# Kernel optimization log

Measured on AMD Instinct MI355X. Metric: run time of the kernel, lower is better.

The kernel has to match this reference:

```python
import jax, jax.numpy as jnp
import numpy as np

B, S, D, E, K, H = 2, 1024, 1024, 8, 2, 2048
Z_COEF = 1e-4  # router_z_loss_coef


def setup_inputs() -> dict:
    key = jax.random.key(0)
    ks = jax.random.split(key, 9)
    std = 0.02
    return {
        "x": jax.random.normal(ks[0], (B, S, D), jnp.float32),
        "router_w": jax.random.normal(ks[1], (E, D), jnp.float32) * std,
        "router_bias": jnp.zeros((E,), jnp.float32),
        "gate_w": jax.random.normal(ks[2], (E, H, D), jnp.float32) * std,
        "up_w": jax.random.normal(ks[3], (E, H, D), jnp.float32) * std,
        "down_w": jax.random.normal(ks[4], (E, D, H), jnp.float32) * std,
        "sh_gate_w": jax.random.normal(ks[5], (H, D), jnp.float32) * std,
        "sh_up_w": jax.random.normal(ks[6], (H, D), jnp.float32) * std,
        "sh_down_w": jax.random.normal(ks[7], (D, H), jnp.float32) * std,
    }


def reference(x, router_w, router_bias, gate_w, up_w, down_w, sh_gate_w, sh_up_w, sh_down_w):
    b, s, d = x.shape
    flat = x.reshape(-1, d)                                   # [N, D]
    n_tokens = flat.shape[0]

    # ---- router ----
    logits = flat @ router_w.T                                # [N, E]
    biased = logits + jax.lax.stop_gradient(router_bias)      # bias is detached
    _, topk_idx = jax.lax.top_k(biased, K)                    # [N, K]
    topk_logits = jnp.take_along_axis(logits, topk_idx, axis=-1)
    topk_weights = jax.nn.softmax(topk_logits.astype(jnp.float32), axis=-1).astype(x.dtype)

    router_z = jax.nn.logsumexp(logits.astype(jnp.float32), axis=-1)
    router_z_loss = jnp.mean(router_z ** 2) * Z_COEF

    # ---- load-balance stats (detached in the original via no_grad) ----
    full_probs = jax.lax.stop_gradient(jax.nn.softmax(logits.astype(jnp.float32), axis=-1))
    p_i = full_probs.mean(axis=0)                             # [E]
    mask = jnp.zeros_like(full_probs).at[jnp.arange(n_tokens)[:, None], topk_idx].set(1.0)
    f_i = mask.mean(axis=0)                                   # [E]
    load_balance = jnp.sum(p_i * f_i) * E
    aux_loss = jnp.zeros((), x.dtype)                         # load_balancing == "aux_loss_free"

    # ---- routed experts ----
    # Identical math to gather(weights)[token] + SwiGLU einsum + scatter-add:
    # out[n] = sum_k w[n,k] * SwiGLU_{idx[n,k]}(x[n]), computed as E masked GEMMs
    # to avoid materializing [N*K, H, D] weight copies.
    routed = jnp.zeros_like(flat)
    for e in range(E):
        w_e = jnp.sum(topk_weights * (topk_idx == e), axis=-1)            # [N]
        h = jax.nn.silu(flat @ gate_w[e].T) * (flat @ up_w[e].T)          # [N, H]
        routed = routed + w_e[:, None] * (h @ down_w[e].T)                # [N, D]

    # ---- shared expert (num_shared_experts = 1) ----
    shared = (jax.nn.silu(flat @ sh_gate_w.T) * (flat @ sh_up_w.T)) @ sh_down_w.T

    hidden_states = (routed + shared).reshape(b, s, d)
    return hidden_states, aux_loss, router_z_loss, jax.lax.stop_gradient(load_balance)
```

## Files before the change

kernel.cpp:

```cpp
#include <hip/hip_runtime.h>

#define N_TOK 2048
#define DIM   1024
#define NE    8
#define HID   2048
#define A_SHARED 4096
#define OUT_HID (N_TOK * DIM)

typedef float v4f __attribute__((ext_vector_type(4)));
typedef short v8s __attribute__((ext_vector_type(8)));

#define OFF_XBF   0ull
#define OFF_H     4194304ull
#define OFF_GW    29360128ull
#define OFF_UW    67108864ull
#define OFF_DW    104857600ull
#define OFF_TOK   142606336ull
#define OFF_WL    (OFF_TOK + 24576ull)
#define OFF_IDX   (OFF_WL + 24576ull)
#define OFF_TW    (OFF_IDX + 16384ull)
#define OFF_STATS (OFF_TW + 16384ull)

struct Stats {
  int counts[NE];
  int fill[NE];
  int offs[NE + 2];
  float z2;
  float psum[NE];
};

__device__ __forceinline__ unsigned short f2bf(float f) {
  union { float f; unsigned u; } v; v.f = f;
  unsigned r = v.u + 0x7FFFu + ((v.u >> 16) & 1u);
  return (unsigned short)(r >> 16);
}
__device__ __forceinline__ unsigned pack2bf(float a, float b) {
  return (unsigned)f2bf(a) | ((unsigned)f2bf(b) << 16);
}

__device__ __forceinline__ void async_lds16(const void* g, void* l) {
  __builtin_amdgcn_global_load_lds(
      (const __attribute__((address_space(1))) void*)g,
      (__attribute__((address_space(3))) void*)l, 16, 0, 0);
}

#define REG_F8 2359296u
#define EXP_F8 2097152u
__global__ __launch_bounds__(256) void cast_w_kernel(
    const float* __restrict__ g, const float* __restrict__ u, const float* __restrict__ dn,
    const float* __restrict__ shg, const float* __restrict__ shu, const float* __restrict__ shd,
    unsigned short* __restrict__ outw) {
  unsigned r = blockIdx.y;
  unsigned j = blockIdx.x * 256 + threadIdx.x;
  const float* eb = (r == 0) ? g : (r == 1) ? u : dn;
  const float* sb = (r == 0) ? shg : (r == 1) ? shu : shd;
  const float* src = (j < EXP_F8) ? eb + 8ull * j : sb + 8ull * (j - EXP_F8);
  float4 a = ((const float4*)src)[0];
  float4 b = ((const float4*)src)[1];
  uint4 o;
  o.x = pack2bf(a.x, a.y);
  o.y = pack2bf(a.z, a.w);
  o.z = pack2bf(b.x, b.y);
  o.w = pack2bf(b.z, b.w);
  ((uint4*)outw)[(size_t)r * REG_F8 + j] = o;
}

__global__ __launch_bounds__(256) void router_kernel(
    const float* __restrict__ x, const float* __restrict__ rw, const float* __restrict__ rb,
    unsigned short* __restrict__ xbf,
    int* __restrict__ idxbuf, float* __restrict__ twbuf, Stats* __restrict__ st) {
  int lane = threadIdx.x & 63;
  int wv = threadIdx.x >> 6;
  int n = blockIdx.x * 4 + wv;

  float acc[NE];
#pragma unroll
  for (int e = 0; e < NE; ++e) acc[e] = 0.f;

  const float4* x4 = (const float4*)(x + (size_t)n * DIM);
  uint2* xb2 = (uint2*)xbf + (size_t)n * 256;
#pragma unroll
  for (int q = 0; q < 4; ++q) {
    float4 xv = x4[q * 64 + lane];
    uint2 xo;
    xo.x = pack2bf(xv.x, xv.y);
    xo.y = pack2bf(xv.z, xv.w);
    xb2[q * 64 + lane] = xo;
#pragma unroll
    for (int e = 0; e < NE; ++e) {
      const float4* w4 = (const float4*)(rw + (size_t)e * DIM);
      float4 wvv = w4[q * 64 + lane];
      acc[e] += xv.x * wvv.x + xv.y * wvv.y + xv.z * wvv.z + xv.w * wvv.w;
    }
  }
#pragma unroll
  for (int off = 32; off; off >>= 1) {
#pragma unroll
    for (int e = 0; e < NE; ++e) acc[e] += __shfl_xor(acc[e], off);
  }

  float mx = acc[0];
#pragma unroll
  for (int e = 1; e < NE; ++e) mx = fmaxf(mx, acc[e]);
  float pr[NE];
  float es = 0.f;
#pragma unroll
  for (int e = 0; e < NE; ++e) { pr[e] = __expf(acc[e] - mx); es += pr[e]; }
  float inv = 1.f / es;
#pragma unroll
  for (int e = 0; e < NE; ++e) pr[e] *= inv;
  float z = mx + __logf(es);

  float b0 = -1e30f; int i0 = 0;
#pragma unroll
  for (int e = 0; e < NE; ++e) {
    float bb = acc[e] + rb[e];
    if (bb > b0) { b0 = bb; i0 = e; }
  }
  float b1 = -1e30f; int i1 = 0;
#pragma unroll
  for (int e = 0; e < NE; ++e) {
    if (e == i0) continue;
    float bb = acc[e] + rb[e];
    if (bb > b1) { b1 = bb; i1 = e; }
  }
  float l0 = acc[i0], l1 = acc[i1];
  float m2 = fmaxf(l0, l1);
  float e0 = __expf(l0 - m2), e1 = __expf(l1 - m2);
  float den = 1.f / (e0 + e1);
  float w0 = e0 * den, w1 = e1 * den;

  __shared__ float redp[4][9];
  __shared__ int redc[4][8];
  if (lane == 0) {
    idxbuf[n * 2] = i0; idxbuf[n * 2 + 1] = i1;
    twbuf[n * 2] = w0;  twbuf[n * 2 + 1] = w1;
#pragma unroll
    for (int e = 0; e < NE; ++e) redp[wv][e] = pr[e];
    redp[wv][8] = z * z;
#pragma unroll
    for (int e = 0; e < NE; ++e) redc[wv][e] = (e == i0) + (e == i1);
  }
  __syncthreads();
  int t = threadIdx.x;
  if (t < 9) {
    float s = redp[0][t] + redp[1][t] + redp[2][t] + redp[3][t];
    if (t < 8) atomicAdd(&st->psum[t], s);
    else       atomicAdd(&st->z2, s);
  } else if (t >= 16 && t < 24) {
    int e = t - 16;
    atomicAdd(&st->counts[e], redc[0][e] + redc[1][e] + redc[2][e] + redc[3][e]);
  }
}

__global__ void scan_kernel(Stats* __restrict__ st, float* __restrict__ out) {
  if (threadIdx.x == 0 && blockIdx.x == 0) {
    int o = 0;
#pragma unroll
    for (int e = 0; e < NE; ++e) { st->offs[e] = o; o += st->counts[e]; }
    st->offs[NE] = o;
    st->offs[NE + 1] = o + N_TOK;
    float zl = st->z2 / (float)N_TOK * 1e-4f;
    float lb = 0.f;
#pragma unroll
    for (int e = 0; e < NE; ++e)
      lb += (st->psum[e] / (float)N_TOK) * ((float)st->counts[e] / (float)N_TOK);
    lb *= (float)NE;
    out[OUT_HID + 0] = 0.f;
    out[OUT_HID + 1] = zl;
    out[OUT_HID + 2] = lb;
  }
}

__global__ __launch_bounds__(256) void scatter_kernel(
    const int* __restrict__ idxbuf, const float* __restrict__ twbuf,
    Stats* __restrict__ st, int* __restrict__ tok, float* __restrict__ wl) {
  int n = blockIdx.x * 256 + threadIdx.x;
#pragma unroll
  for (int k = 0; k < 2; ++k) {
    int e = idxbuf[n * 2 + k];
    int pos = st->offs[e] + atomicAdd(&st->fill[e], 1);
    tok[pos] = n;
    wl[pos] = twbuf[n * 2 + k];
  }
  tok[A_SHARED + n] = n;
  wl[A_SHARED + n] = 1.f;
}


__global__ __launch_bounds__(256, 2) void gateup_kernel(
    const unsigned short* __restrict__ gwbf, const unsigned short* __restrict__ uwbf,
    const unsigned short* __restrict__ xbf, const int* __restrict__ tok,
    const Stats* __restrict__ st, unsigned short* __restrict__ hbuf) {
  int e = blockIdx.z;
  int seg0 = st->offs[e];
  int cnt = st->offs[e + 1] - seg0;
  int m0 = blockIdx.y * 128;
  if (m0 >= cnt) return;
  int n0 = blockIdx.x * 128;

  __shared__ alignas(16) unsigned short As[2][128 * 32];
  __shared__ alignas(16) unsigned short Bg[2][128 * 32];
  __shared__ alignas(16) unsigned short Bu[2][128 * 32];

  int tid = threadIdx.x, l = tid & 63, w = tid >> 6;
  int wr = w >> 1, wc = w & 1;

  int sj = l >> 3;
  int ss = (l & 7) ^ sj;
  int grow = 2 * sj + (ss >> 2);
  int gch = ss & 3;

  const unsigned short* ap[2];
  const unsigned short* gp[2];
  const unsigned short* up[2];
#pragma unroll
  for (int q = 0; q < 2; ++q) {
    int row = (w * 2 + q) * 16 + grow;
    int ar = m0 + row; if (ar > cnt - 1) ar = cnt - 1;
    ap[q] = xbf + (size_t)tok[seg0 + ar] * DIM + gch * 8;
    size_t wb = (size_t)e * HID * DIM + (size_t)(n0 + row) * DIM + gch * 8;
    gp[q] = gwbf + wb;
    up[q] = uwbf + wb;
  }

  int lh = (l & 15) >> 1;
  int lofs = lh * 64 + ((((l & 1) * 4 + (l >> 4)) ^ lh) * 8);

  v4f accg[4][4], accu[4][4];
#pragma unroll
  for (int mi = 0; mi < 4; ++mi)
#pragma unroll
    for (int ni = 0; ni < 4; ++ni) {
      accg[mi][ni] = (v4f){0.f, 0.f, 0.f, 0.f};
      accu[mi][ni] = (v4f){0.f, 0.f, 0.f, 0.f};
    }

#pragma unroll
  for (int q = 0; q < 2; ++q) {
    async_lds16(ap[q], &As[0][(w * 2 + q) * 512]);
    async_lds16(gp[q], &Bg[0][(w * 2 + q) * 512]);
    async_lds16(up[q], &Bu[0][(w * 2 + q) * 512]);
  }

  int pb = 0;
  for (int k0 = 0; k0 < DIM; k0 += 32, pb ^= 1) {
    __syncthreads();

    v8s af[4], bgf[4], buf_[4];
#pragma unroll
    for (int mi = 0; mi < 4; ++mi)
      af[mi] = *(const v8s*)&As[pb][(wr * 32 + mi * 8) * 64 + lofs];
#pragma unroll
    for (int ni = 0; ni < 4; ++ni) {
      bgf[ni]  = *(const v8s*)&Bg[pb][(wc * 32 + ni * 8) * 64 + lofs];
      buf_[ni] = *(const v8s*)&Bu[pb][(wc * 32 + ni * 8) * 64 + lofs];
    }

    if (k0 + 32 < DIM) {
      int nb = pb ^ 1;
      int kn = k0 + 32;
#pragma unroll
      for (int q = 0; q < 2; ++q) {
        async_lds16(ap[q] + kn, &As[nb][(w * 2 + q) * 512]);
        async_lds16(gp[q] + kn, &Bg[nb][(w * 2 + q) * 512]);
        async_lds16(up[q] + kn, &Bu[nb][(w * 2 + q) * 512]);
      }
    }

#pragma unroll
    for (int mi = 0; mi < 4; ++mi)
#pragma unroll
      for (int ni = 0; ni < 4; ++ni) {
        accg[mi][ni] = __builtin_amdgcn_mfma_f32_16x16x32_bf16(af[mi], bgf[ni], accg[mi][ni], 0, 0, 0);
        accu[mi][ni] = __builtin_amdgcn_mfma_f32_16x16x32_bf16(af[mi], buf_[ni], accu[mi][ni], 0, 0, 0);
      }
  }

  int col = l & 15, rq = (l >> 4) * 4;
#pragma unroll
  for (int mi = 0; mi < 4; ++mi) {
#pragma unroll
    for (int rr = 0; rr < 4; ++rr) {
      int rl = wr * 64 + mi * 16 + rq + rr;
      if (m0 + rl < cnt) {
        size_t rowb = (size_t)(seg0 + m0 + rl) * HID + n0 + wc * 64;
#pragma unroll
        for (int ni = 0; ni < 4; ++ni) {
          float g = accg[mi][ni][rr], u = accu[mi][ni][rr];
          hbuf[rowb + ni * 16 + col] = f2bf(g * u / (1.f + __expf(-g)));
        }
      }
    }
  }
}

__global__ __launch_bounds__(256, 2) void down_kernel(
    const unsigned short* __restrict__ dwbf, const unsigned short* __restrict__ hbuf,
    const int* __restrict__ tok, const float* __restrict__ wl,
    const Stats* __restrict__ st, float* __restrict__ out) {
  int e = blockIdx.z;
  int seg0 = st->offs[e];
  int cnt = st->offs[e + 1] - seg0;
  int m0 = blockIdx.y * 128;
  if (m0 >= cnt) return;
  int n0 = blockIdx.x * 128;

  __shared__ alignas(16) unsigned short As[2][128 * 32];
  __shared__ alignas(16) unsigned short Bs[2][128 * 32];

  int tid = threadIdx.x, l = tid & 63, w = tid >> 6;
  int wr = w >> 1, wc = w & 1;

  int sj = l >> 3;
  int ss = (l & 7) ^ sj;
  int grow = 2 * sj + (ss >> 2);
  int gch = ss & 3;

  const unsigned short* ap[2];
  const unsigned short* bp[2];
#pragma unroll
  for (int q = 0; q < 2; ++q) {
    int row = (w * 2 + q) * 16 + grow;
    int ar = m0 + row; if (ar > cnt - 1) ar = cnt - 1;
    ap[q] = hbuf + (size_t)(seg0 + ar) * HID + gch * 8;
    bp[q] = dwbf + (size_t)e * DIM * HID + (size_t)(n0 + row) * HID + gch * 8;
  }

  int lh = (l & 15) >> 1;
  int lofs = lh * 64 + ((((l & 1) * 4 + (l >> 4)) ^ lh) * 8);

  v4f acc[4][4];
#pragma unroll
  for (int mi = 0; mi < 4; ++mi)
#pragma unroll
    for (int ni = 0; ni < 4; ++ni) acc[mi][ni] = (v4f){0.f, 0.f, 0.f, 0.f};

#pragma unroll
  for (int q = 0; q < 2; ++q) {
    async_lds16(ap[q], &As[0][(w * 2 + q) * 512]);
    async_lds16(bp[q], &Bs[0][(w * 2 + q) * 512]);
  }

  int pb = 0;
  for (int k0 = 0; k0 < HID; k0 += 32, pb ^= 1) {
    __syncthreads();

    v8s af[4], bf[4];
#pragma unroll
    for (int mi = 0; mi < 4; ++mi)
      af[mi] = *(const v8s*)&As[pb][(wr * 32 + mi * 8) * 64 + lofs];
#pragma unroll
    for (int ni = 0; ni < 4; ++ni)
      bf[ni] = *(const v8s*)&Bs[pb][(wc * 32 + ni * 8) * 64 + lofs];

    if (k0 + 32 < HID) {
      int nb = pb ^ 1;
      int kn = k0 + 32;
#pragma unroll
      for (int q = 0; q < 2; ++q) {
        async_lds16(ap[q] + kn, &As[nb][(w * 2 + q) * 512]);
        async_lds16(bp[q] + kn, &Bs[nb][(w * 2 + q) * 512]);
      }
    }

#pragma unroll
    for (int mi = 0; mi < 4; ++mi)
#pragma unroll
      for (int ni = 0; ni < 4; ++ni)
        acc[mi][ni] = __builtin_amdgcn_mfma_f32_16x16x32_bf16(af[mi], bf[ni], acc[mi][ni], 0, 0, 0);
  }

  int col = l & 15, rq = (l >> 4) * 4;
#pragma unroll
  for (int mi = 0; mi < 4; ++mi) {
#pragma unroll
    for (int rr = 0; rr < 4; ++rr) {
      int rl = wr * 64 + mi * 16 + rq + rr;
      if (m0 + rl < cnt) {
        int t = tok[seg0 + m0 + rl];
        float wgt = wl[seg0 + m0 + rl];
        float* ob = out + (size_t)t * DIM + n0 + wc * 64;
#pragma unroll
        for (int ni = 0; ni < 4; ++ni)
          atomicAdd(ob + ni * 16 + col, acc[mi][ni][rr] * wgt);
      }
    }
  }
}

extern "C" void kernel_launch(void* const* d_in, const int* in_sizes, int n_in,
                              void* d_out, int out_size, void* d_ws, size_t ws_size,
                              hipStream_t stream) {
  const float* x   = (const float*)d_in[0];
  const float* rw  = (const float*)d_in[1];
  const float* rb  = (const float*)d_in[2];
  const float* gw  = (const float*)d_in[3];
  const float* uw  = (const float*)d_in[4];
  const float* dw  = (const float*)d_in[5];
  const float* shg = (const float*)d_in[6];
  const float* shu = (const float*)d_in[7];
  const float* shd = (const float*)d_in[8];
  float* out = (float*)d_out;
  char* ws = (char*)d_ws;

  unsigned short* xbf  = (unsigned short*)(ws + OFF_XBF);
  unsigned short* hbuf = (unsigned short*)(ws + OFF_H);
  unsigned short* gwbf = (unsigned short*)(ws + OFF_GW);
  unsigned short* uwbf = (unsigned short*)(ws + OFF_UW);
  unsigned short* dwbf = (unsigned short*)(ws + OFF_DW);
  int*   tok  = (int*)(ws + OFF_TOK);
  float* wl   = (float*)(ws + OFF_WL);
  int*   idxb = (int*)(ws + OFF_IDX);
  float* twb  = (float*)(ws + OFF_TW);
  Stats* st   = (Stats*)(ws + OFF_STATS);

  hipMemsetAsync(d_out, 0, (size_t)out_size * sizeof(float), stream);
  hipMemsetAsync(st, 0, sizeof(Stats), stream);

  cast_w_kernel<<<dim3(9216, 3), 256, 0, stream>>>(gw, uw, dw, shg, shu, shd, gwbf);
  router_kernel<<<512, 256, 0, stream>>>(x, rw, rb, xbf, idxb, twb, st);
  scan_kernel<<<1, 64, 0, stream>>>(st, out);
  scatter_kernel<<<8, 256, 0, stream>>>(idxb, twb, st, tok, wl);
  gateup_kernel<<<dim3(16, 16, 9), 256, 0, stream>>>(gwbf, uwbf, xbf, tok, st, hbuf);
  down_kernel<<<dim3(8, 16, 9), 256, 0, stream>>>(dwbf, hbuf, tok, wl, st, out);
}
```

Measured before the change: 418.1 us.

## Fuse fp32-to-bf16 weight cast into GEMM tile loads, drop cast kernel

```diff
diff --git a/kernel.cpp b/kernel.cpp
--- a/kernel.cpp
+++ b/kernel.cpp
@@ -12,10 +12,7 @@
 
 #define OFF_XBF   0ull
 #define OFF_H     4194304ull
-#define OFF_GW    29360128ull
-#define OFF_UW    67108864ull
-#define OFF_DW    104857600ull
-#define OFF_TOK   142606336ull
+#define OFF_TOK   29360128ull
 #define OFF_WL    (OFF_TOK + 24576ull)
 #define OFF_IDX   (OFF_WL + 24576ull)
 #define OFF_TW    (OFF_IDX + 16384ull)
@@ -38,31 +35,24 @@
   return (unsigned)f2bf(a) | ((unsigned)f2bf(b) << 16);
 }
 
+__device__ __forceinline__ unsigned cvt2bf(float a, float b) {
+  unsigned r;
+  asm("v_cvt_pk_bf16_f32 %0, %1, %2" : "=v"(r) : "v"(a), "v"(b));
+  return r;
+}
+__device__ __forceinline__ void st8bf(unsigned short* p, float4 a, float4 b) {
+  uint4 o;
+  o.x = cvt2bf(a.x, a.y);
+  o.y = cvt2bf(a.z, a.w);
+  o.z = cvt2bf(b.x, b.y);
+  o.w = cvt2bf(b.z, b.w);
+  *(uint4*)p = o;
+}
+
 __device__ __forceinline__ void async_lds16(const void* g, void* l) {
   __builtin_amdgcn_global_load_lds(
       (const __attribute__((address_space(1))) void*)g,
       (__attribute__((address_space(3))) void*)l, 16, 0, 0);
-}
-
-#define REG_F8 2359296u
-#define EXP_F8 2097152u
-__global__ __launch_bounds__(256) void cast_w_kernel(
-    const float* __restrict__ g, const float* __restrict__ u, const float* __restrict__ dn,
-    const float* __restrict__ shg, const float* __restrict__ shu, const float* __restrict__ shd,
-    unsigned short* __restrict__ outw) {
-  unsigned r = blockIdx.y;
-  unsigned j = blockIdx.x * 256 + threadIdx.x;
-  const float* eb = (r == 0) ? g : (r == 1) ? u : dn;
-  const float* sb = (r == 0) ? shg : (r == 1) ? shu : shd;
-  const float* src = (j < EXP_F8) ? eb + 8ull * j : sb + 8ull * (j - EXP_F8);
-  float4 a = ((const float4*)src)[0];
-  float4 b = ((const float4*)src)[1];
-  uint4 o;
-  o.x = pack2bf(a.x, a.y);
-  o.y = pack2bf(a.z, a.w);
-  o.z = pack2bf(b.x, b.y);
-  o.w = pack2bf(b.z, b.w);
-  ((uint4*)outw)[(size_t)r * REG_F8 + j] = o;
 }
 
 __global__ __launch_bounds__(256) void router_kernel(
@@ -189,7 +179,8 @@
 
 
 __global__ __launch_bounds__(256, 2) void gateup_kernel(
-    const unsigned short* __restrict__ gwbf, const unsigned short* __restrict__ uwbf,
+    const float* __restrict__ gw, const float* __restrict__ uw,
+    const float* __restrict__ shg, const float* __restrict__ shu,
     const unsigned short* __restrict__ xbf, const int* __restrict__ tok,
     const Stats* __restrict__ st, unsigned short* __restrict__ hbuf) {
   int e = blockIdx.z;
@@ -211,17 +202,20 @@
   int grow = 2 * sj + (ss >> 2);
   int gch = ss & 3;
 
+  const float* gbase = (e < NE) ? gw + (size_t)e * HID * DIM : shg;
+  const float* ubase = (e < NE) ? uw + (size_t)e * HID * DIM : shu;
+
   const unsigned short* ap[2];
-  const unsigned short* gp[2];
-  const unsigned short* up[2];
+  const float* gp[2];
+  const float* up[2];
 #pragma unroll
   for (int q = 0; q < 2; ++q) {
     int row = (w * 2 + q) * 16 + grow;
     int ar = m0 + row; if (ar > cnt - 1) ar = cnt - 1;
     ap[q] = xbf + (size_t)tok[seg0 + ar] * DIM + gch * 8;
-    size_t wb = (size_t)e * HID * DIM + (size_t)(n0 + row) * DIM + gch * 8;
-    gp[q] = gwbf + wb;
-    up[q] = uwbf + wb;
+    size_t wb = (size_t)(n0 + row) * DIM + gch * 8;
+    gp[q] = gbase + wb;
+    up[q] = ubase + wb;
   }
 
   int lh = (l & 15) >> 1;
@@ -236,11 +230,21 @@
       accu[mi][ni] = (v4f){0.f, 0.f, 0.f, 0.f};
     }
 
+  float4 rg[2][2], ru[2][2];
 #pragma unroll
   for (int q = 0; q < 2; ++q) {
+    rg[q][0] = ((const float4*)gp[q])[0];
+    rg[q][1] = ((const float4*)gp[q])[1];
+    ru[q][0] = ((const float4*)up[q])[0];
+    ru[q][1] = ((const float4*)up[q])[1];
+  }
+#pragma unroll
+  for (int q = 0; q < 2; ++q)
     async_lds16(ap[q], &As[0][(w * 2 + q) * 512]);
-    async_lds16(gp[q], &Bg[0][(w * 2 + q) * 512]);
-    async_lds16(up[q], &Bu[0][(w * 2 + q) * 512]);
+#pragma unroll
+  for (int q = 0; q < 2; ++q) {
+    st8bf(&Bg[0][(w * 2 + q) * 512 + l * 8], rg[q][0], rg[q][1]);
+    st8bf(&Bu[0][(w * 2 + q) * 512 + l * 8], ru[q][0], ru[q][1]);
   }
 
   int pb = 0;
@@ -257,15 +261,19 @@
       buf_[ni] = *(const v8s*)&Bu[pb][(wc * 32 + ni * 8) * 64 + lofs];
     }
 
-    if (k0 + 32 < DIM) {
-      int nb = pb ^ 1;
-      int kn = k0 + 32;
+    int nb = pb ^ 1;
+    int kn = k0 + 32;
+    if (kn < DIM) {
 #pragma unroll
       for (int q = 0; q < 2; ++q) {
+        rg[q][0] = ((const float4*)(gp[q] + kn))[0];
+        rg[q][1] = ((const float4*)(gp[q] + kn))[1];
+        ru[q][0] = ((const float4*)(up[q] + kn))[0];
+        ru[q][1] = ((const float4*)(up[q] + kn))[1];
+      }
+#pragma unroll
+      for (int q = 0; q < 2; ++q)
         async_lds16(ap[q] + kn, &As[nb][(w * 2 + q) * 512]);
-        async_lds16(gp[q] + kn, &Bg[nb][(w * 2 + q) * 512]);
-        async_lds16(up[q] + kn, &Bu[nb][(w * 2 + q) * 512]);
-      }
     }
 
 #pragma unroll
@@ -275,6 +283,14 @@
         accg[mi][ni] = __builtin_amdgcn_mfma_f32_16x16x32_bf16(af[mi], bgf[ni], accg[mi][ni], 0, 0, 0);
         accu[mi][ni] = __builtin_amdgcn_mfma_f32_16x16x32_bf16(af[mi], buf_[ni], accu[mi][ni], 0, 0, 0);
       }
+
+    if (kn < DIM) {
+#pragma unroll
+      for (int q = 0; q < 2; ++q) {
+        st8bf(&Bg[nb][(w * 2 + q) * 512 + l * 8], rg[q][0], rg[q][1]);
+        st8bf(&Bu[nb][(w * 2 + q) * 512 + l * 8], ru[q][0], ru[q][1]);
+      }
+    }
   }
 
   int col = l & 15, rq = (l >> 4) * 4;
@@ -296,7 +312,8 @@
 }
 
 __global__ __launch_bounds__(256, 2) void down_kernel(
-    const unsigned short* __restrict__ dwbf, const unsigned short* __restrict__ hbuf,
+    const float* __restrict__ dw, const float* __restrict__ shd,
+    const unsigned short* __restrict__ hbuf,
     const int* __restrict__ tok, const float* __restrict__ wl,
     const Stats* __restrict__ st, float* __restrict__ out) {
   int e = blockIdx.z;
@@ -317,14 +334,16 @@
   int grow = 2 * sj + (ss >> 2);
   int gch = ss & 3;
 
+  const float* dbase = (e < NE) ? dw + (size_t)e * DIM * HID : shd;
+
   const unsigned short* ap[2];
-  const unsigned short* bp[2];
+  const float* bp[2];
 #pragma unroll
   for (int q = 0; q < 2; ++q) {
     int row = (w * 2 + q) * 16 + grow;
     int ar = m0 + row; if (ar > cnt - 1) ar = cnt - 1;
     ap[q] = hbuf + (size_t)(seg0 + ar) * HID + gch * 8;
-    bp[q] = dwbf + (size_t)e * DIM * HID + (size_t)(n0 + row) * HID + gch * 8;
+    bp[q] = dbase + (size_t)(n0 + row) * HID + gch * 8;
   }
 
   int lh = (l & 15) >> 1;
@@ -336,11 +355,18 @@
 #pragma unroll
     for (int ni = 0; ni < 4; ++ni) acc[mi][ni] = (v4f){0.f, 0.f, 0.f, 0.f};
 
+  float4 rb_[2][2];
 #pragma unroll
   for (int q = 0; q < 2; ++q) {
+    rb_[q][0] = ((const float4*)bp[q])[0];
+    rb_[q][1] = ((const float4*)bp[q])[1];
+  }
+#pragma unroll
+  for (int q = 0; q < 2; ++q)
     async_lds16(ap[q], &As[0][(w * 2 + q) * 512]);
-    async_lds16(bp[q], &Bs[0][(w * 2 + q) * 512]);
-  }
+#pragma unroll
+  for (int q = 0; q < 2; ++q)
+    st8bf(&Bs[0][(w * 2 + q) * 512 + l * 8], rb_[q][0], rb_[q][1]);
 
   int pb = 0;
   for (int k0 = 0; k0 < HID; k0 += 32, pb ^= 1) {
@@ -354,14 +380,17 @@
     for (int ni = 0; ni < 4; ++ni)
       bf[ni] = *(const v8s*)&Bs[pb][(wc * 32 + ni * 8) * 64 + lofs];
 
-    if (k0 + 32 < HID) {
-      int nb = pb ^ 1;
-      int kn = k0 + 32;
+    int nb = pb ^ 1;
+    int kn = k0 + 32;
+    if (kn < HID) {
 #pragma unroll
       for (int q = 0; q < 2; ++q) {
+        rb_[q][0] = ((const float4*)(bp[q] + kn))[0];
+        rb_[q][1] = ((const float4*)(bp[q] + kn))[1];
+      }
+#pragma unroll
+      for (int q = 0; q < 2; ++q)
         async_lds16(ap[q] + kn, &As[nb][(w * 2 + q) * 512]);
-        async_lds16(bp[q] + kn, &Bs[nb][(w * 2 + q) * 512]);
-      }
     }
 
 #pragma unroll
@@ -369,6 +398,12 @@
 #pragma unroll
       for (int ni = 0; ni < 4; ++ni)
         acc[mi][ni] = __builtin_amdgcn_mfma_f32_16x16x32_bf16(af[mi], bf[ni], acc[mi][ni], 0, 0, 0);
+
+    if (kn < HID) {
+#pragma unroll
+      for (int q = 0; q < 2; ++q)
+        st8bf(&Bs[nb][(w * 2 + q) * 512 + l * 8], rb_[q][0], rb_[q][1]);
+    }
   }
 
   int col = l & 15, rq = (l >> 4) * 4;
@@ -406,9 +441,6 @@
 
   unsigned short* xbf  = (unsigned short*)(ws + OFF_XBF);
   unsigned short* hbuf = (unsigned short*)(ws + OFF_H);
-  unsigned short* gwbf = (unsigned short*)(ws + OFF_GW);
-  unsigned short* uwbf = (unsigned short*)(ws + OFF_UW);
-  unsigned short* dwbf = (unsigned short*)(ws + OFF_DW);
   int*   tok  = (int*)(ws + OFF_TOK);
   float* wl   = (float*)(ws + OFF_WL);
   int*   idxb = (int*)(ws + OFF_IDX);
@@ -418,10 +450,9 @@
   hipMemsetAsync(d_out, 0, (size_t)out_size * sizeof(float), stream);
   hipMemsetAsync(st, 0, sizeof(Stats), stream);
 
-  cast_w_kernel<<<dim3(9216, 3), 256, 0, stream>>>(gw, uw, dw, shg, shu, shd, gwbf);
   router_kernel<<<512, 256, 0, stream>>>(x, rw, rb, xbf, idxb, twb, st);
   scan_kernel<<<1, 64, 0, stream>>>(st, out);
   scatter_kernel<<<8, 256, 0, stream>>>(idxb, twb, st, tok, wl);
-  gateup_kernel<<<dim3(16, 16, 9), 256, 0, stream>>>(gwbf, uwbf, xbf, tok, st, hbuf);
-  down_kernel<<<dim3(8, 16, 9), 256, 0, stream>>>(dwbf, hbuf, tok, wl, st, out);
-}
+  gateup_kernel<<<dim3(16, 16, 9), 256, 0, stream>>>(gw, uw, shg, shu, xbf, tok, st, hbuf);
+  down_kernel<<<dim3(8, 16, 9), 256, 0, stream>>>(dw, shd, hbuf, tok, wl, st, out);
+}
```

Result: slower. 446.9 us (+6.9%).
